# Kernel optimization log

Hardware: AMD Instinct MI355X
Metric: run time of the kernel (lower is better)

## Reference

```python
import jax, jax.numpy as jnp
import numpy as np

S, T, N, D, H, DT = 4, 4, 65536, 128, 128, 128


def setup_inputs() -> dict:
    key = jax.random.key(0)
    ks = jax.random.split(key, 9)
    inv_d = 1.0 / np.sqrt(D)
    inv_h = 1.0 / np.sqrt(H)
    return {
        "states": jax.random.normal(ks[0], (N, D), dtype=jnp.float32),
        "scores": jax.random.uniform(ks[1], (N, 1), dtype=jnp.float32),
        "type_ids": jax.random.randint(ks[2], (N,), 0, S, dtype=jnp.int32),
        "type_matching": jax.random.normal(ks[3], (S, T), dtype=jnp.float32),
        "W1": jax.random.normal(ks[4], (S, T, D, H), dtype=jnp.float32) * inv_d,
        "b1": jnp.zeros((S, T, H), dtype=jnp.float32),
        "W2": jax.random.normal(ks[5], (S, T, H, DT), dtype=jnp.float32) * inv_h,
        "b2": jnp.zeros((S, T, DT), dtype=jnp.float32),
        "C1": jax.random.normal(ks[6], (S, T, D, H), dtype=jnp.float32) * inv_d,
        "c1": jnp.zeros((S, T, H), dtype=jnp.float32),
        "C2": jax.random.normal(ks[7], (S, T, H, 1), dtype=jnp.float32) * inv_h,
        "c2": jnp.zeros((S, T, 1), dtype=jnp.float32),
    }


def reference(states, scores, type_ids, type_matching, W1, b1, W2, b2, C1, c1, C2, c2):
    """Batched MetaphorMorphism.forward with best_match_only=True.

    For each item with source type s: route to t* = argmax sigmoid(type_matching[s]),
    apply mapper MLP (D->H->DT, ReLU), classifier MLP (D->H->1, ReLU, sigmoid),
    new_score = min(score, classifier_out), item_prob = sigmoid(type_matching)[s, t*].
    """
    match_sig = jax.nn.sigmoid(type_matching)          # [S, T]
    best_t = jnp.argmax(type_matching, axis=1)         # [S] (argmax of sigmoid == argmax of logits)
    best_prob = match_sig[jnp.arange(S), best_t]       # [S]

    out_state = jnp.zeros((states.shape[0], W2.shape[-1]), dtype=states.dtype)
    out_score = jnp.zeros_like(scores)
    # loop over the small, fixed set of source types (structurally distinct experts)
    for s in range(S):
        t = best_t[s]
        h = jax.nn.relu(states @ W1[s, t] + b1[s, t])          # [N, H]
        y = h @ W2[s, t] + b2[s, t]                            # [N, DT]
        hc = jax.nn.relu(states @ C1[s, t] + c1[s, t])         # [N, H]
        cls = jax.nn.sigmoid(hc @ C2[s, t] + c2[s, t])         # [N, 1]
        new_score = jnp.minimum(scores, cls)                   # [N, 1]
        m = (type_ids == s)[:, None]
        out_state = jnp.where(m, y, out_state)
        out_score = jnp.where(m, new_score, out_score)
    item_prob = best_prob[type_ids]                            # [N]
    return out_state, out_score, item_prob
```

## Files before the change

kernel.cpp:

```cpp
#include <hip/hip_runtime.h>
#include <math.h>

#define Nn 65536

typedef short s16x8 __attribute__((ext_vector_type(8)));
typedef float f32x4 __attribute__((ext_vector_type(4)));
typedef unsigned int u32;

__device__ __forceinline__ unsigned short f2bf(float x) {
    u32 u = __float_as_uint(x);
    u += 0x7FFFu + ((u >> 16) & 1u);
    return (unsigned short)(u >> 16);
}

__device__ __forceinline__ int best_t_for(const float* __restrict__ tm, int s, float* mOut) {
    float m = tm[s * 4];
    int am = 0;
#pragma unroll
    for (int j = 1; j < 4; ++j) {
        float v = tm[s * 4 + j];
        if (v > m) { m = v; am = j; }
    }
    if (mOut) *mOut = m;
    return am;
}

__global__ void k_prepw(const float* __restrict__ tm,
                        const float* __restrict__ W1, const float* __restrict__ W2,
                        const float* __restrict__ C1, unsigned short* __restrict__ wbf) {
    int u = blockIdx.x * 256 + threadIdx.x;
    int mat = u >> 11;
    int rr = u & 2047;
    int f = rr >> 6, lane = rr & 63;
    int kk = f >> 3, n8 = f & 7;
    int q = lane >> 4, l15 = lane & 15;
    int sm = mat / 3, w = mat - sm * 3;
    int t = best_t_for(tm, sm, nullptr);
    const float* src = (w == 0) ? W1 : (w == 1) ? W2 : C1;
    const float* sp = src + (((sm * 4 + t) << 14) + n8 * 16 + l15);
    int k0 = kk * 32 + q * 8;
    s16x8 o;
#pragma unroll
    for (int j = 0; j < 8; ++j) o[j] = (short)f2bf(sp[(k0 + j) * 128]);
    *(s16x8*)(wbf + (size_t)u * 8) = o;
}

__global__ __launch_bounds__(512, 4) void k_fused(
    const float* __restrict__ states, const float* __restrict__ scores,
    const int* __restrict__ type_ids, const float* __restrict__ tm,
    const float* __restrict__ b1g, const float* __restrict__ b2g,
    const float* __restrict__ c1g, const float* __restrict__ C2,
    const float* __restrict__ c2, const unsigned short* __restrict__ wbf,
    float* __restrict__ out_state, float* __restrict__ out_score,
    float* __restrict__ out_prob)
{
    __shared__ __align__(16) unsigned short Abuf[64 * 128];
    __shared__ __align__(16) unsigned short Hbuf[112 * 128];
    __shared__ int permLds[112];
    __shared__ int segTypeLds[8];
    __shared__ int Gs;
    __shared__ float scoreLds[64];
    __shared__ float pLds[8][112];
    __shared__ float c2sL[4];

    const int t = threadIdx.x;
    const int gid0 = blockIdx.x * 64;
    const int lane = t & 63;
    const int wv = t >> 6;
    const int l15 = lane & 15;
    const int quad = lane >> 4;
    const int myRow = t >> 3;
    const int q8 = t & 7;
    const int col = wv * 16 + l15;

    int stIdx4[4];
#pragma unroll
    for (int s = 0; s < 4; ++s) stIdx4[s] = s * 4 + best_t_for(tm, s, nullptr);
    float b1vA[4], b2vA[4], c1vA[4], c2wA[4];
#pragma unroll
    for (int s = 0; s < 4; ++s) {
        b1vA[s] = b1g[stIdx4[s] * 128 + col];
        b2vA[s] = b2g[stIdx4[s] * 128 + col];
        c1vA[s] = c1g[stIdx4[s] * 128 + col];
        c2wA[s] = C2[stIdx4[s] * 128 + col];
    }
    if (t < 4) c2sL[t] = c2[stIdx4[t]];

    {
        const int g = gid0 + myRow;
        const float4* sp = (const float4*)(states + (size_t)g * 128 + q8 * 16);
        float4 v[4];
#pragma unroll
        for (int i = 0; i < 4; ++i) v[i] = sp[i];
        unsigned short* dstRow = &Abuf[myRow * 128];
        const int rot = (myRow & 15) << 3;
#pragma unroll
        for (int i = 0; i < 4; ++i) {
            int c = (q8 * 16 + i * 4 + rot) & 127;
            ushort4 o;
            o.x = f2bf(v[i].x); o.y = f2bf(v[i].y);
            o.z = f2bf(v[i].z); o.w = f2bf(v[i].w);
            *(ushort4*)(dstRow + c) = o;
        }
    }

    if (t < 64) {
        int ty = type_ids[gid0 + t];
        scoreLds[t] = scores[gid0 + t];
        float m = tm[ty * 4];
#pragma unroll
        for (int j = 1; j < 4; ++j) m = fmaxf(m, tm[ty * 4 + j]);
        out_prob[gid0 + t] = 1.f / (1.f + expf(-m));

        unsigned long long m0 = __ballot(ty == 0);
        unsigned long long m1 = __ballot(ty == 1);
        unsigned long long m2 = __ballot(ty == 2);
        unsigned long long m3 = __ballot(ty == 3);
        int c0 = (int)__popcll(m0), c1 = (int)__popcll(m1);
        int c2_ = (int)__popcll(m2), c3 = (int)__popcll(m3);
        int ns0 = (c0 + 15) >> 4, ns1 = (c1 + 15) >> 4;
        int ns2 = (c2_ + 15) >> 4, ns3 = (c3 + 15) >> 4;
        int pb1 = ns0 * 16, pb2 = pb1 + ns1 * 16, pb3 = pb2 + ns2 * 16;
        permLds[t] = -1;
        if (t < 48) permLds[64 + t] = -1;
        unsigned long long lt = (1ull << t) - 1ull;
        int pb = (ty == 0) ? 0 : (ty == 1) ? pb1 : (ty == 2) ? pb2 : pb3;
        unsigned long long mm = (ty == 0) ? m0 : (ty == 1) ? m1 : (ty == 2) ? m2 : m3;
        permLds[pb + (int)__popcll(mm & lt)] = t;
        if (t < 8) {
            int st = (t < ns0) ? 0 : (t < ns0 + ns1) ? 1 : (t < ns0 + ns1 + ns2) ? 2 : 3;
            segTypeLds[t] = st;
        }
        if (t == 0) Gs = ns0 + ns1 + ns2 + ns3;
    }
    __syncthreads();
    const int G = Gs;

    const unsigned short* __restrict__ wbase = wbf;
    auto loadWf = [&](int m, int sty, s16x8 wf[4]) {
        const unsigned short* wb = wbase + ((size_t)sty * 3 + m) * 16384;
#pragma unroll
        for (int kk = 0; kk < 4; ++kk)
            wf[kk] = *(const s16x8*)(wb + (size_t)((kk * 8 + wv) * 64 + lane) * 8);
    };
    auto gemmA = [&](int g, const s16x8 wf[4]) -> f32x4 {
        f32x4 acc = {0.f, 0.f, 0.f, 0.f};
        int pRow = permLds[g * 16 + l15];
        int rbase = ((pRow >= 0) ? pRow : 0) * 128;
        int rot = (pRow & 15) << 3;
#pragma unroll
        for (int kk = 0; kk < 4; ++kk) {
            s16x8 af = *(const s16x8*)(Abuf + rbase + ((kk * 32 + quad * 8 + rot) & 127));
            if (pRow < 0) af = s16x8{0, 0, 0, 0, 0, 0, 0, 0};
            acc = __builtin_amdgcn_mfma_f32_16x16x32_bf16(af, wf[kk], acc, 0, 0, 0);
        }
        return acc;
    };
    auto gemmH = [&](int g, const s16x8 wf[4]) -> f32x4 {
        f32x4 acc = {0.f, 0.f, 0.f, 0.f};
        const unsigned short* hb = Hbuf + (g * 16 + l15) * 128;
#pragma unroll
        for (int kk = 0; kk < 4; ++kk) {
            s16x8 af = *(const s16x8*)(hb + ((kk * 32 + quad * 8 + (l15 << 3)) & 127));
            acc = __builtin_amdgcn_mfma_f32_16x16x32_bf16(af, wf[kk], acc, 0, 0, 0);
        }
        return acc;
    };

    s16x8 wfP[2][4];

    loadWf(0, segTypeLds[0], wfP[0]);
#pragma unroll
    for (int g = 0; g < 7; ++g) {
        if (g < G) {
            if (g + 1 < G) loadWf(0, segTypeLds[g + 1], wfP[(g + 1) & 1]);
            f32x4 a = gemmA(g, wfP[g & 1]);
            int sty = segTypeLds[g];
            float bb = (sty == 0) ? b1vA[0] : (sty == 1) ? b1vA[1] : (sty == 2) ? b1vA[2] : b1vA[3];
#pragma unroll
            for (int r = 0; r < 4; ++r) {
                int row = g * 16 + quad * 4 + r;
                float v = fmaxf(a[r] + bb, 0.f);
                Hbuf[row * 128 + ((col + ((row & 15) << 3)) & 127)] = f2bf(v);
            }
        }
    }
    __syncthreads();

    loadWf(1, segTypeLds[0], wfP[0]);
#pragma unroll
    for (int g = 0; g < 7; ++g) {
        if (g < G) {
            if (g + 1 < G) loadWf(1, segTypeLds[g + 1], wfP[(g + 1) & 1]);
            f32x4 a = gemmH(g, wfP[g & 1]);
            int sty = segTypeLds[g];
            float bb = (sty == 0) ? b2vA[0] : (sty == 1) ? b2vA[1] : (sty == 2) ? b2vA[2] : b2vA[3];
#pragma unroll
            for (int r = 0; r < 4; ++r) {
                int p = permLds[g * 16 + quad * 4 + r];
                if (p >= 0) out_state[(size_t)(gid0 + p) * 128 + col] = a[r] + bb;
            }
        }
    }

    loadWf(2, segTypeLds[0], wfP[0]);
#pragma unroll
    for (int g = 0; g < 7; ++g) {
        if (g < G) {
            if (g + 1 < G) loadWf(2, segTypeLds[g + 1], wfP[(g + 1) & 1]);
            f32x4 a = gemmA(g, wfP[g & 1]);
            int sty = segTypeLds[g];
            float cv = (sty == 0) ? c1vA[0] : (sty == 1) ? c1vA[1] : (sty == 2) ? c1vA[2] : c1vA[3];
            float cw = (sty == 0) ? c2wA[0] : (sty == 1) ? c2wA[1] : (sty == 2) ? c2wA[2] : c2wA[3];
            float part[4];
#pragma unroll
            for (int r = 0; r < 4; ++r) part[r] = fmaxf(a[r] + cv, 0.f) * cw;
#pragma unroll
            for (int off = 1; off < 16; off <<= 1)
#pragma unroll
                for (int r = 0; r < 4; ++r) part[r] += __shfl_xor(part[r], off, 64);
            if (l15 == 0) {
#pragma unroll
                for (int r = 0; r < 4; ++r) pLds[wv][g * 16 + quad * 4 + r] = part[r];
            }
        }
    }
    __syncthreads();

    if (t < 112 && t < G * 16) {
        int p = permLds[t];
        if (p >= 0) {
            float tot = pLds[0][t] + pLds[1][t] + pLds[2][t] + pLds[3][t]
                      + pLds[4][t] + pLds[5][t] + pLds[6][t] + pLds[7][t]
                      + c2sL[segTypeLds[t >> 4]];
            float cls = 1.f / (1.f + expf(-tot));
            out_score[gid0 + p] = fminf(scoreLds[p], cls);
        }
    }
}

extern "C" void kernel_launch(void* const* d_in, const int* in_sizes, int n_in,
                              void* d_out, int out_size, void* d_ws, size_t ws_size,
                              hipStream_t stream) {
    const float* states = (const float*)d_in[0];
    const float* scores = (const float*)d_in[1];
    const int*   type_ids = (const int*)d_in[2];
    const float* tm = (const float*)d_in[3];
    const float* W1 = (const float*)d_in[4];
    const float* b1 = (const float*)d_in[5];
    const float* W2 = (const float*)d_in[6];
    const float* b2 = (const float*)d_in[7];
    const float* C1 = (const float*)d_in[8];
    const float* c1 = (const float*)d_in[9];
    const float* C2 = (const float*)d_in[10];
    const float* c2 = (const float*)d_in[11];

    unsigned short* wbf = (unsigned short*)d_ws;

    float* out_state = (float*)d_out;
    float* out_score = out_state + (size_t)Nn * 128;
    float* out_prob  = out_score + Nn;

    k_prepw<<<96, 256, 0, stream>>>(tm, W1, W2, C1, wbf);
    k_fused<<<1024, 512, 0, stream>>>(states, scores, type_ids, tm, b1, b2, c1,
        C2, c2, wbf, out_state, out_score, out_prob);
}
```

Baseline: 136.1 us.

## Process 128 rows per block and loop per type to reuse weight fragments

Each block now handles 128 rows instead of 64, which halves the grid and spreads each type's weight-fragment load over more row segments. The segment loop is restructured to iterate by type, loading W1/W2/C1 fragments once per type rather than double-buffering per segment. Classifier partial sums are accumulated with LDS atomics, and out_prob is computed in the final epilogue. The price is more LDS per block (lower occupancy), an extra barrier per type, and no overlap between weight loads and MFMA work.

Result: faster. 128.6 us (-5.5%).

```diff
diff --git a/kernel.cpp b/kernel.cpp
--- a/kernel.cpp
+++ b/kernel.cpp
@@ -54,49 +54,40 @@
     float* __restrict__ out_state, float* __restrict__ out_score,
     float* __restrict__ out_prob)
 {
-    __shared__ __align__(16) unsigned short Abuf[64 * 128];
-    __shared__ __align__(16) unsigned short Hbuf[112 * 128];
-    __shared__ int permLds[112];
-    __shared__ int segTypeLds[8];
-    __shared__ int Gs;
-    __shared__ float scoreLds[64];
-    __shared__ float pLds[8][112];
-    __shared__ float c2sL[4];
+    __shared__ __align__(16) unsigned short Abuf[128 * 128];
+    __shared__ __align__(16) unsigned short Hbuf[176 * 128];
+    __shared__ int permLds[176];
+    __shared__ float pSum[176];
+    __shared__ int wcnt[2][4];
 
     const int t = threadIdx.x;
-    const int gid0 = blockIdx.x * 64;
+    const int gid0 = blockIdx.x * 128;
     const int lane = t & 63;
     const int wv = t >> 6;
     const int l15 = lane & 15;
     const int quad = lane >> 4;
-    const int myRow = t >> 3;
-    const int q8 = t & 7;
+    const int myRow = t >> 2;
+    const int q4 = t & 3;
     const int col = wv * 16 + l15;
 
     int stIdx4[4];
-#pragma unroll
-    for (int s = 0; s < 4; ++s) stIdx4[s] = s * 4 + best_t_for(tm, s, nullptr);
-    float b1vA[4], b2vA[4], c1vA[4], c2wA[4];
-#pragma unroll
-    for (int s = 0; s < 4; ++s) {
-        b1vA[s] = b1g[stIdx4[s] * 128 + col];
-        b2vA[s] = b2g[stIdx4[s] * 128 + col];
-        c1vA[s] = c1g[stIdx4[s] * 128 + col];
-        c2wA[s] = C2[stIdx4[s] * 128 + col];
-    }
-    if (t < 4) c2sL[t] = c2[stIdx4[t]];
+    float bmax[4];
+#pragma unroll
+    for (int s = 0; s < 4; ++s) stIdx4[s] = s * 4 + best_t_for(tm, s, &bmax[s]);
+
+    if (t < 176) { permLds[t] = -1; pSum[t] = 0.f; }
 
     {
         const int g = gid0 + myRow;
-        const float4* sp = (const float4*)(states + (size_t)g * 128 + q8 * 16);
-        float4 v[4];
-#pragma unroll
-        for (int i = 0; i < 4; ++i) v[i] = sp[i];
+        const float4* sp = (const float4*)(states + (size_t)g * 128 + q4 * 32);
+        float4 v[8];
+#pragma unroll
+        for (int i = 0; i < 8; ++i) v[i] = sp[i];
         unsigned short* dstRow = &Abuf[myRow * 128];
         const int rot = (myRow & 15) << 3;
 #pragma unroll
-        for (int i = 0; i < 4; ++i) {
-            int c = (q8 * 16 + i * 4 + rot) & 127;
+        for (int i = 0; i < 8; ++i) {
+            int c = (q4 * 32 + i * 4 + rot) & 127;
             ushort4 o;
             o.x = f2bf(v[i].x); o.y = f2bf(v[i].y);
             o.z = f2bf(v[i].z); o.w = f2bf(v[i].w);
@@ -104,61 +95,63 @@
         }
     }
 
-    if (t < 64) {
-        int ty = type_ids[gid0 + t];
-        scoreLds[t] = scores[gid0 + t];
-        float m = tm[ty * 4];
-#pragma unroll
-        for (int j = 1; j < 4; ++j) m = fmaxf(m, tm[ty * 4 + j]);
-        out_prob[gid0 + t] = 1.f / (1.f + expf(-m));
-
-        unsigned long long m0 = __ballot(ty == 0);
-        unsigned long long m1 = __ballot(ty == 1);
-        unsigned long long m2 = __ballot(ty == 2);
-        unsigned long long m3 = __ballot(ty == 3);
-        int c0 = (int)__popcll(m0), c1 = (int)__popcll(m1);
-        int c2_ = (int)__popcll(m2), c3 = (int)__popcll(m3);
-        int ns0 = (c0 + 15) >> 4, ns1 = (c1 + 15) >> 4;
-        int ns2 = (c2_ + 15) >> 4, ns3 = (c3 + 15) >> 4;
-        int pb1 = ns0 * 16, pb2 = pb1 + ns1 * 16, pb3 = pb2 + ns2 * 16;
-        permLds[t] = -1;
-        if (t < 48) permLds[64 + t] = -1;
-        unsigned long long lt = (1ull << t) - 1ull;
-        int pb = (ty == 0) ? 0 : (ty == 1) ? pb1 : (ty == 2) ? pb2 : pb3;
-        unsigned long long mm = (ty == 0) ? m0 : (ty == 1) ? m1 : (ty == 2) ? m2 : m3;
-        permLds[pb + (int)__popcll(mm & lt)] = t;
-        if (t < 8) {
-            int st = (t < ns0) ? 0 : (t < ns0 + ns1) ? 1 : (t < ns0 + ns1 + ns2) ? 2 : 3;
-            segTypeLds[t] = st;
-        }
-        if (t == 0) Gs = ns0 + ns1 + ns2 + ns3;
+    int myty = 0, w2 = 0;
+    unsigned long long msk = 0;
+    if (t < 128) {
+        w2 = t >> 6;
+        myty = type_ids[gid0 + t];
+#pragma unroll
+        for (int sv = 0; sv < 4; ++sv) {
+            unsigned long long mm = __ballot(myty == sv);
+            if (myty == sv) msk = mm;
+            if (lane == 0) wcnt[w2][sv] = (int)__popcll(mm);
+        }
     }
     __syncthreads();
-    const int G = Gs;
+
+    int nsA[4], sbA[4], G;
+    {
+        int sb = 0;
+#pragma unroll
+        for (int sv = 0; sv < 4; ++sv) {
+            int c = wcnt[0][sv] + wcnt[1][sv];
+            nsA[sv] = (c + 15) >> 4;
+            sbA[sv] = sb;
+            sb += nsA[sv];
+        }
+        G = sb;
+    }
+    if (t < 128) {
+        unsigned long long lt = (1ull << lane) - 1ull;
+        int pos = sbA[myty] * 16 + ((w2 == 1) ? wcnt[0][myty] : 0) + (int)__popcll(msk & lt);
+        permLds[pos] = t;
+    }
+    __syncthreads();
 
     const unsigned short* __restrict__ wbase = wbf;
-    auto loadWf = [&](int m, int sty, s16x8 wf[4]) {
-        const unsigned short* wb = wbase + ((size_t)sty * 3 + m) * 16384;
+    s16x8 wf[4];
+    auto loadWf = [&](int ty, int m) {
+        const unsigned short* wb = wbase + ((size_t)ty * 3 + m) * 16384;
 #pragma unroll
         for (int kk = 0; kk < 4; ++kk)
             wf[kk] = *(const s16x8*)(wb + (size_t)((kk * 8 + wv) * 64 + lane) * 8);
     };
-    auto gemmA = [&](int g, const s16x8 wf[4]) -> f32x4 {
+    auto gemmA = [&](int seg) -> f32x4 {
         f32x4 acc = {0.f, 0.f, 0.f, 0.f};
-        int pRow = permLds[g * 16 + l15];
-        int rbase = ((pRow >= 0) ? pRow : 0) * 128;
-        int rot = (pRow & 15) << 3;
+        int pRow = permLds[seg * 16 + l15];
+        int rr = (pRow >= 0) ? pRow : 0;
+        const int rbase = rr * 128;
+        const int rot = (rr & 15) << 3;
 #pragma unroll
         for (int kk = 0; kk < 4; ++kk) {
             s16x8 af = *(const s16x8*)(Abuf + rbase + ((kk * 32 + quad * 8 + rot) & 127));
-            if (pRow < 0) af = s16x8{0, 0, 0, 0, 0, 0, 0, 0};
             acc = __builtin_amdgcn_mfma_f32_16x16x32_bf16(af, wf[kk], acc, 0, 0, 0);
         }
         return acc;
     };
-    auto gemmH = [&](int g, const s16x8 wf[4]) -> f32x4 {
+    auto gemmH = [&](int seg) -> f32x4 {
         f32x4 acc = {0.f, 0.f, 0.f, 0.f};
-        const unsigned short* hb = Hbuf + (g * 16 + l15) * 128;
+        const unsigned short* hb = Hbuf + (seg * 16 + l15) * 128;
 #pragma unroll
         for (int kk = 0; kk < 4; ++kk) {
             s16x8 af = *(const s16x8*)(hb + ((kk * 32 + quad * 8 + (l15 << 3)) & 127));
@@ -167,74 +160,76 @@
         return acc;
     };
 
-    s16x8 wfP[2][4];
-
-    loadWf(0, segTypeLds[0], wfP[0]);
-#pragma unroll
-    for (int g = 0; g < 7; ++g) {
-        if (g < G) {
-            if (g + 1 < G) loadWf(0, segTypeLds[g + 1], wfP[(g + 1) & 1]);
-            f32x4 a = gemmA(g, wfP[g & 1]);
-            int sty = segTypeLds[g];
-            float bb = (sty == 0) ? b1vA[0] : (sty == 1) ? b1vA[1] : (sty == 2) ? b1vA[2] : b1vA[3];
-#pragma unroll
-            for (int r = 0; r < 4; ++r) {
-                int row = g * 16 + quad * 4 + r;
-                float v = fmaxf(a[r] + bb, 0.f);
-                Hbuf[row * 128 + ((col + ((row & 15) << 3)) & 127)] = f2bf(v);
+    for (int ty = 0; ty < 4; ++ty) {
+        const int ns = nsA[ty];
+        if (ns == 0) continue;
+        const int sb = sbA[ty];
+        const int si0 = stIdx4[ty];
+
+        loadWf(ty, 0);
+        {
+            const float b1v = b1g[si0 * 128 + col];
+            for (int si = 0; si < ns; ++si) {
+                const int seg = sb + si;
+                f32x4 a = gemmA(seg);
+#pragma unroll
+                for (int r = 0; r < 4; ++r) {
+                    int row = seg * 16 + quad * 4 + r;
+                    float v = fmaxf(a[r] + b1v, 0.f);
+                    Hbuf[row * 128 + ((col + ((row & 15) << 3)) & 127)] = f2bf(v);
+                }
             }
         }
+        __syncthreads();
+
+        loadWf(ty, 1);
+        {
+            const float b2v = b2g[si0 * 128 + col];
+            for (int si = 0; si < ns; ++si) {
+                const int seg = sb + si;
+                f32x4 a = gemmH(seg);
+#pragma unroll
+                for (int r = 0; r < 4; ++r) {
+                    int p = permLds[seg * 16 + quad * 4 + r];
+                    if (p >= 0) out_state[(size_t)(gid0 + p) * 128 + col] = a[r] + b2v;
+                }
+            }
+        }
+
+        loadWf(ty, 2);
+        {
+            const float c1v = c1g[si0 * 128 + col];
+            const float c2w = C2[si0 * 128 + col];
+            for (int si = 0; si < ns; ++si) {
+                const int seg = sb + si;
+                f32x4 a = gemmA(seg);
+                float part[4];
+#pragma unroll
+                for (int r = 0; r < 4; ++r) part[r] = fmaxf(a[r] + c1v, 0.f) * c2w;
+#pragma unroll
+                for (int off = 1; off < 16; off <<= 1)
+#pragma unroll
+                    for (int r = 0; r < 4; ++r)
+                        part[r] += __shfl_xor(part[r], off, 64);
+                if (l15 == 0) {
+#pragma unroll
+                    for (int r = 0; r < 4; ++r)
+                        atomicAdd(&pSum[seg * 16 + quad * 4 + r], part[r]);
+                }
+            }
+        }
     }
     __syncthreads();
 
-    loadWf(1, segTypeLds[0], wfP[0]);
-#pragma unroll
-    for (int g = 0; g < 7; ++g) {
-        if (g < G) {
-            if (g + 1 < G) loadWf(1, segTypeLds[g + 1], wfP[(g + 1) & 1]);
-            f32x4 a = gemmH(g, wfP[g & 1]);
-            int sty = segTypeLds[g];
-            float bb = (sty == 0) ? b2vA[0] : (sty == 1) ? b2vA[1] : (sty == 2) ? b2vA[2] : b2vA[3];
-#pragma unroll
-            for (int r = 0; r < 4; ++r) {
-                int p = permLds[g * 16 + quad * 4 + r];
-                if (p >= 0) out_state[(size_t)(gid0 + p) * 128 + col] = a[r] + bb;
-            }
-        }
-    }
-
-    loadWf(2, segTypeLds[0], wfP[0]);
-#pragma unroll
-    for (int g = 0; g < 7; ++g) {
-        if (g < G) {
-            if (g + 1 < G) loadWf(2, segTypeLds[g + 1], wfP[(g + 1) & 1]);
-            f32x4 a = gemmA(g, wfP[g & 1]);
-            int sty = segTypeLds[g];
-            float cv = (sty == 0) ? c1vA[0] : (sty == 1) ? c1vA[1] : (sty == 2) ? c1vA[2] : c1vA[3];
-            float cw = (sty == 0) ? c2wA[0] : (sty == 1) ? c2wA[1] : (sty == 2) ? c2wA[2] : c2wA[3];
-            float part[4];
-#pragma unroll
-            for (int r = 0; r < 4; ++r) part[r] = fmaxf(a[r] + cv, 0.f) * cw;
-#pragma unroll
-            for (int off = 1; off < 16; off <<= 1)
-#pragma unroll
-                for (int r = 0; r < 4; ++r) part[r] += __shfl_xor(part[r], off, 64);
-            if (l15 == 0) {
-#pragma unroll
-                for (int r = 0; r < 4; ++r) pLds[wv][g * 16 + quad * 4 + r] = part[r];
-            }
-        }
-    }
-    __syncthreads();
-
-    if (t < 112 && t < G * 16) {
+    if (t < G * 16) {
         int p = permLds[t];
         if (p >= 0) {
-            float tot = pLds[0][t] + pLds[1][t] + pLds[2][t] + pLds[3][t]
-                      + pLds[4][t] + pLds[5][t] + pLds[6][t] + pLds[7][t]
-                      + c2sL[segTypeLds[t >> 4]];
+            int seg = t >> 4;
+            int sty = (seg >= sbA[1] ? 1 : 0) + (seg >= sbA[2] ? 1 : 0) + (seg >= sbA[3] ? 1 : 0);
+            float tot = pSum[t] + c2[stIdx4[sty]];
             float cls = 1.f / (1.f + expf(-tot));
-            out_score[gid0 + p] = fminf(scoreLds[p], cls);
+            out_score[gid0 + p] = fminf(scores[gid0 + p], cls);
+            out_prob[gid0 + p] = 1.f / (1.f + expf(-bmax[sty]));
         }
     }
 }
@@ -262,6 +257,6 @@
     float* out_prob  = out_score + Nn;
 
     k_prepw<<<96, 256, 0, stream>>>(tm, W1, W2, C1, wbf);
-    k_fused<<<1024, 512, 0, stream>>>(states, scores, type_ids, tm, b1, b2, c1,
+    k_fused<<<512, 512, 0, stream>>>(states, scores, type_ids, tm, b1, b2, c1,
         C2, c2, wbf, out_state, out_score, out_prob);
 }
```
